# Optimization experiments

Measured on AMD Instinct MI355X. Metric: run time of the kernel, lower is better.

## Reference

```python
import jax, jax.numpy as jnp
import numpy as np

B, T, D = 2, 2048, 1024
H, KVH = 16, 4
HD = D // H            # 64
HALF = HD // 2         # 32
DFF = 4096
KW = 15
EPS = 1e-6


def zcrms(x, scale):
    # zero-centred RMSNorm: (1 + scale) * x / rms(x)
    rms = jnp.sqrt(jnp.mean(jnp.square(x.astype(jnp.float32)), axis=-1, keepdims=True) + EPS)
    return ((1.0 + scale) * x / rms).astype(x.dtype)


def apply_rope(x, cos, sin):
    # x: [B, H, T, HD]; cos/sin: [T, HALF]
    c = cos[None, None, :, :]
    s = sin[None, None, :, :]
    x1, x2 = x[..., :HALF], x[..., HALF:]
    return jnp.concatenate([x1 * c - x2 * s, x2 * c + x1 * s], axis=-1)


def setup_inputs() -> dict:
    key = jax.random.key(0)
    ks = jax.random.split(key, 20)
    std = 0.02
    inp = {
        "x": jax.random.normal(ks[0], (B, T, D), jnp.float32),
        "mask": jnp.ones((1, 1, T, T), dtype=bool),
        "cos": jnp.cos(jnp.arange(T, dtype=jnp.float32)[:, None]
                       * (10000.0 ** (-jnp.arange(HALF, dtype=jnp.float32) / HALF))[None, :]),
        "sin": jnp.sin(jnp.arange(T, dtype=jnp.float32)[:, None]
                       * (10000.0 ** (-jnp.arange(HALF, dtype=jnp.float32) / HALF))[None, :]),
        # attention
        "attn_norm_scale": jax.random.normal(ks[1], (D,), jnp.float32) * std,
        "q_kernel": jax.random.normal(ks[2], (D, D), jnp.float32) * std,
        "k_kernel": jax.random.normal(ks[3], (D, KVH * HD), jnp.float32) * std,
        "v_kernel": jax.random.normal(ks[4], (D, KVH * HD), jnp.float32) * std,
        "q_norm_scale": jax.random.normal(ks[5], (HD,), jnp.float32) * std,
        "k_norm_scale": jax.random.normal(ks[6], (HD,), jnp.float32) * std,
        "o_kernel": jax.random.normal(ks[7], (D, D), jnp.float32) * std,
        # conv module
        "conv_norm_scale": jax.random.normal(ks[8], (D,), jnp.float32) * std,
        "pw_up_kernel": jax.random.normal(ks[9], (D, 2 * D), jnp.float32) * std,
        "dw_kernel": jax.random.normal(ks[10], (KW, 1, D), jnp.float32) * std,
        "conv_inner_norm_scale": jax.random.normal(ks[11], (D,), jnp.float32) * std,
        "pw_down_kernel": jax.random.normal(ks[12], (D, D), jnp.float32) * std,
        # ffn
        "ffn_norm_scale": jax.random.normal(ks[13], (D,), jnp.float32) * std,
        "gate_kernel": jax.random.normal(ks[14], (D, DFF), jnp.float32) * std,
        "up_kernel": jax.random.normal(ks[15], (D, DFF), jnp.float32) * std,
        "down_kernel": jax.random.normal(ks[16], (DFF, D), jnp.float32) * std,
    }
    return inp


def reference(x, mask, cos, sin, attn_norm_scale, q_kernel, k_kernel, v_kernel,
              q_norm_scale, k_norm_scale, o_kernel, conv_norm_scale, pw_up_kernel,
              dw_kernel, conv_inner_norm_scale, pw_down_kernel, ffn_norm_scale,
              gate_kernel, up_kernel, down_kernel):
    # ---- pre-norm self-attention (GQA + QK-RMSNorm + RoPE) ----
    h = zcrms(x, attn_norm_scale)
    q = (h @ q_kernel).reshape(B, T, H, HD).transpose(0, 2, 1, 3)      # [B,H,T,HD]
    k = (h @ k_kernel).reshape(B, T, KVH, HD).transpose(0, 2, 1, 3)    # [B,KVH,T,HD]
    v = (h @ v_kernel).reshape(B, T, KVH, HD).transpose(0, 2, 1, 3)
    q = zcrms(q, q_norm_scale)
    k = zcrms(k, k_norm_scale)
    rep = H // KVH
    k = jnp.repeat(k, rep, axis=1)
    v = jnp.repeat(v, rep, axis=1)
    q = apply_rope(q, cos, sin)
    k = apply_rope(k, cos, sin)
    scale = jnp.sqrt(jnp.float32(HD))
    aw = jnp.einsum('bhqd,bhkd->bhqk', q, k) / scale
    aw = jnp.where(mask, aw, jnp.finfo(aw.dtype).min)
    aw = jax.nn.softmax(aw, axis=-1)
    attn = jnp.einsum('bhqk,bhkd->bhqd', aw, v).transpose(0, 2, 1, 3).reshape(B, T, D)
    x = x + attn @ o_kernel

    # ---- conformer conv module: pw_up -> GLU -> depthwise conv -> norm -> pw_down ----
    h = zcrms(x, conv_norm_scale)
    u = h @ pw_up_kernel
    u1, u2 = jnp.split(u, 2, axis=-1)
    g = u1 * jax.nn.sigmoid(u2)                                        # [B,T,D]
    c = jax.lax.conv_general_dilated(
        g, dw_kernel, window_strides=(1,), padding='SAME',
        feature_group_count=D, dimension_numbers=('NWC', 'WIO', 'NWC'))
    c = zcrms(c, conv_inner_norm_scale)
    x = x + c @ pw_down_kernel

    # ---- gated FFN with drelu activation ----
    h = zcrms(x, ffn_norm_scale)
    ff = jax.nn.relu(h @ gate_kernel) * jax.nn.relu(h @ up_kernel)
    x = x + ff @ down_kernel
    return x
```

## Files before the change

kernel.cpp:

```cpp
#include <hip/hip_runtime.h>


#define TT   2048
#define NTOK 4096

typedef __attribute__((ext_vector_type(8))) short short8;
typedef __attribute__((ext_vector_type(4))) float floatx4;

__device__ __forceinline__ unsigned short f2bf(float f) {
  unsigned int u = __float_as_uint(f);
  u = (u + 0x7fffu + ((u >> 16) & 1u)) >> 16;
  return (unsigned short)u;
}
__device__ __forceinline__ float bf2f(unsigned short s) {
  return __uint_as_float(((unsigned int)s) << 16);
}

__device__ __forceinline__ void glds16(const void* g, void* lds_base) {
  __builtin_amdgcn_global_load_lds(
      (const __attribute__((address_space(1))) void*)g,
      (__attribute__((address_space(3))) void*)lds_base, 16, 0, 0);
}

struct WJobs {
  const float* src[9];
  unsigned short* dst[9];
  int K[9], M[9], pm[9];
  int start[10];
};

__global__ __launch_bounds__(256) void wconv_all_kernel(WJobs tab) {
  int b = blockIdx.x;
  int j = 0;
  while (b >= tab.start[j + 1]) j++;
  int t = b - tab.start[j];
  const float* src = tab.src[j];
  unsigned short* dst = tab.dst[j];
  int K = tab.K[j], M = tab.M[j], pm = tab.pm[j];
  int mt = M >> 5;
  int m0 = (t % mt) * 32, k0 = (t / mt) * 32;
  int rowbase;
  if (pm == 0)      rowbase = m0;
  else if (pm == 1) rowbase = ((m0 & 1023) >> 5) * 64 + (m0 >> 10) * 32;
  else if (pm == 2) rowbase = (m0 >> 5) * 64;
  else              rowbase = (m0 >> 5) * 64 + 32;
  __shared__ float tile[32][33];
  int tx = threadIdx.x & 31, ty = threadIdx.x >> 5;
  for (int r = ty; r < 32; r += 8)
    tile[r][tx] = src[(size_t)(k0 + r) * M + m0 + tx];
  __syncthreads();
  for (int r = ty; r < 32; r += 8)
    dst[(size_t)(rowbase + r) * K + k0 + tx] = f2bf(tile[tx][r]);
}

template <bool BF16IN>
__global__ __launch_bounds__(256) void rmsnorm_kernel(
    const void* __restrict__ xin, const float* __restrict__ scale,
    unsigned short* __restrict__ out) {
  int t = blockIdx.x, tid = threadIdx.x;
  float xv[4];
  if (BF16IN) {
    ushort4 u = ((const ushort4*)((const unsigned short*)xin + (size_t)t * 1024))[tid];
    xv[0] = bf2f(u.x); xv[1] = bf2f(u.y); xv[2] = bf2f(u.z); xv[3] = bf2f(u.w);
  } else {
    float4 u = ((const float4*)((const float*)xin + (size_t)t * 1024))[tid];
    xv[0] = u.x; xv[1] = u.y; xv[2] = u.z; xv[3] = u.w;
  }
  float ss = xv[0] * xv[0] + xv[1] * xv[1] + xv[2] * xv[2] + xv[3] * xv[3];
#pragma unroll
  for (int off = 32; off > 0; off >>= 1) ss += __shfl_down(ss, off);
  __shared__ float red[4];
  if ((tid & 63) == 0) red[tid >> 6] = ss;
  __syncthreads();
  float rinv = rsqrtf((red[0] + red[1] + red[2] + red[3]) * (1.0f / 1024.0f) + 1e-6f);
  float4 sv = ((const float4*)scale)[tid];
  ushort4 o;
  o.x = f2bf((1.0f + sv.x) * xv[0] * rinv);
  o.y = f2bf((1.0f + sv.y) * xv[1] * rinv);
  o.z = f2bf((1.0f + sv.z) * xv[2] * rinv);
  o.w = f2bf((1.0f + sv.w) * xv[3] * rinv);
  ((ushort4*)(out + (size_t)t * 1024))[tid] = o;
}

template <int BN, int FUSE, int OUT, int RES>
__device__ __forceinline__ void gemm_body(
    const unsigned short* __restrict__ A, const unsigned short* __restrict__ Bt,
    void* __restrict__ Cout, const void* __restrict__ resid, int K, int M) {
  constexpr int NI = BN / 32;
  __shared__ __align__(16) unsigned short As[128 * 64];
  __shared__ __align__(16) unsigned short Bs[BN * 64];
  const int tid = threadIdx.x;
  const int wid = tid >> 6, lane = tid & 63;
  const int quad = lane >> 4, l16 = lane & 15;
  const int wm = (wid >> 1) * 64, wn = (wid & 1) * (BN / 2);

  int bx = blockIdx.x, by = blockIdx.y;
  if (gridDim.x == 16) {
    int pid = by * gridDim.x + bx;
    int inb = pid & 63, pidp = pid >> 6;
    by = (pidp & 3) * 8 + (inb & 7);
    bx = (pidp >> 2) * 8 + (inb >> 3);
  }
  const int row0 = by * 128;
  const int col0 = bx * BN;

  floatx4 acc[4][NI];
#pragma unroll
  for (int mi = 0; mi < 4; mi++)
#pragma unroll
    for (int ni = 0; ni < NI; ni++) acc[mi][ni] = (floatx4){0.f, 0.f, 0.f, 0.f};

  const unsigned short* Ag = A + (size_t)row0 * K;
  const unsigned short* Bg = Bt + (size_t)col0 * K;

  for (int k0 = 0; k0 < K; k0 += 64) {
#pragma unroll
    for (int j = 0; j < 4; j++) {
      int ci = tid + j * 256;
      int r = ci >> 3, c = (ci & 7) ^ (r & 7);
      glds16(Ag + (size_t)r * K + k0 + c * 8, &As[(wid * 64 + j * 256) * 8]);
    }
#pragma unroll
    for (int j = 0; j < BN / 32; j++) {
      int ci = tid + j * 256;
      int r = ci >> 3, c = (ci & 7) ^ (r & 7);
      glds16(Bg + (size_t)r * K + k0 + c * 8, &Bs[(wid * 64 + j * 256) * 8]);
    }
    __syncthreads();
#pragma unroll
    for (int kk = 0; kk < 64; kk += 32) {
      short8 a[4], b[NI];
#pragma unroll
      for (int mi = 0; mi < 4; mi++) {
        int r = wm + mi * 16 + l16;
        a[mi] = *(const short8*)&As[r * 64 + (((kk >> 3) + quad) ^ (r & 7)) * 8];
      }
#pragma unroll
      for (int ni = 0; ni < NI; ni++) {
        int r = wn + ni * 16 + l16;
        b[ni] = *(const short8*)&Bs[r * 64 + (((kk >> 3) + quad) ^ (r & 7)) * 8];
      }
#pragma unroll
      for (int mi = 0; mi < 4; mi++)
#pragma unroll
        for (int ni = 0; ni < NI; ni++)
          acc[mi][ni] = __builtin_amdgcn_mfma_f32_16x16x32_bf16(a[mi], b[ni], acc[mi][ni], 0, 0, 0);
    }
    __syncthreads();
  }

  if (FUSE == 0) {
#pragma unroll
    for (int mi = 0; mi < 4; mi++) {
#pragma unroll
      for (int reg = 0; reg < 4; reg++) {
        int grow = row0 + wm + mi * 16 + quad * 4 + reg;
#pragma unroll
        for (int ni = 0; ni < NI; ni++) {
          int gcol = col0 + wn + ni * 16 + l16;
          float v = acc[mi][ni][reg];
          if (RES == 1) v += ((const float*)resid)[(size_t)grow * M + gcol];
          if (RES == 2) v += bf2f(((const unsigned short*)resid)[(size_t)grow * M + gcol]);
          if (OUT == 1) ((unsigned short*)Cout)[(size_t)grow * M + gcol] = f2bf(v);
          else          ((float*)Cout)[(size_t)grow * M + gcol] = v;
        }
      }
    }
  } else {
    const int group = (col0 + wn) >> 6;
    const int MW = M >> 1;
#pragma unroll
    for (int mi = 0; mi < 4; mi++) {
#pragma unroll
      for (int reg = 0; reg < 4; reg++) {
        int grow = row0 + wm + mi * 16 + quad * 4 + reg;
#pragma unroll
        for (int ni = 0; ni < NI / 2; ni++) {
          int f = group * 32 + ni * 16 + l16;
          float a = acc[mi][ni][reg], b = acc[mi][ni + NI / 2][reg];
          float v;
          if (FUSE == 1) v = a / (1.0f + __expf(-b));
          else           v = fmaxf(a, 0.f) * fmaxf(b, 0.f);
          ((unsigned short*)Cout)[(size_t)grow * MW + f] = f2bf(v);
        }
      }
    }
  }
}

__global__ __launch_bounds__(256, 2) void gemm_oproj(
    const unsigned short* A, const unsigned short* Bt, void* C, const void* r, int K, int M) {
  gemm_body<64, 0, 1, 1>(A, Bt, C, r, K, M);
}
__global__ __launch_bounds__(256, 2) void gemm_glu(
    const unsigned short* A, const unsigned short* Bt, void* C, const void* r, int K, int M) {
  gemm_body<128, 1, 1, 0>(A, Bt, C, r, K, M);
}
__global__ __launch_bounds__(256, 2) void gemm_dn(
    const unsigned short* A, const unsigned short* Bt, void* C, const void* r, int K, int M) {
  gemm_body<64, 0, 1, 2>(A, Bt, C, r, K, M);
}
__global__ __launch_bounds__(256, 2) void gemm_gateup(
    const unsigned short* A, const unsigned short* Bt, void* C, const void* r, int K, int M) {
  gemm_body<128, 2, 1, 0>(A, Bt, C, r, K, M);
}
__global__ __launch_bounds__(256, 2) void gemm_ffdn(
    const unsigned short* A, const unsigned short* Bt, void* C, const void* r, int K, int M) {
  gemm_body<64, 0, 0, 2>(A, Bt, C, r, K, M);
}

#define QSCALE 0.180336880111f

__global__ __launch_bounds__(256, 2) void gemm_qkvf(
    const unsigned short* __restrict__ A, const unsigned short* __restrict__ Bt,
    const float* __restrict__ cosb, const float* __restrict__ sinb,
    const float* __restrict__ qns, const float* __restrict__ kns,
    unsigned short* __restrict__ qb, unsigned short* __restrict__ kb,
    unsigned short* __restrict__ vt) {
  constexpr int K = 1024;
  __shared__ __align__(16) unsigned short As[128 * 64];
  __shared__ __align__(16) unsigned short Bs[128 * 64];
  const int tid = threadIdx.x;
  const int wid = tid >> 6, lane = tid & 63;
  const int quad = lane >> 4, l16 = lane & 15;
  const int wm = (wid >> 1) * 64, wn = (wid & 1) * 64;
  const int row0 = blockIdx.y * 128;
  const int col0 = blockIdx.x * 128;

  floatx4 acc[4][4];
#pragma unroll
  for (int mi = 0; mi < 4; mi++)
#pragma unroll
    for (int ni = 0; ni < 4; ni++) acc[mi][ni] = (floatx4){0.f, 0.f, 0.f, 0.f};

  const unsigned short* Ag = A + (size_t)row0 * K;
  const unsigned short* Bg = Bt + (size_t)col0 * K;

  for (int k0 = 0; k0 < K; k0 += 64) {
#pragma unroll
    for (int j = 0; j < 4; j++) {
      int ci = tid + j * 256;
      int r = ci >> 3, c = (ci & 7) ^ (r & 7);
      glds16(Ag + (size_t)r * K + k0 + c * 8, &As[(wid * 64 + j * 256) * 8]);
      glds16(Bg + (size_t)r * K + k0 + c * 8, &Bs[(wid * 64 + j * 256) * 8]);
    }
    __syncthreads();
#pragma unroll
    for (int kk = 0; kk < 64; kk += 32) {
      short8 a[4], b[4];
#pragma unroll
      for (int mi = 0; mi < 4; mi++) {
        int r = wm + mi * 16 + l16;
        a[mi] = *(const short8*)&As[r * 64 + (((kk >> 3) + quad) ^ (r & 7)) * 8];
      }
#pragma unroll
      for (int ni = 0; ni < 4; ni++) {
        int r = wn + ni * 16 + l16;
        b[ni] = *(const short8*)&Bs[r * 64 + (((kk >> 3) + quad) ^ (r & 7)) * 8];
      }
#pragma unroll
      for (int mi = 0; mi < 4; mi++)
#pragma unroll
        for (int ni = 0; ni < 4; ni++)
          acc[mi][ni] = __builtin_amdgcn_mfma_f32_16x16x32_bf16(a[mi], b[ni], acc[mi][ni], 0, 0, 0);
    }
    __syncthreads();
  }

  const int head = (col0 + wn) >> 6;
  const int bi = row0 >> 11;

  if (head < 20) {
    const float* ns = (head < 16) ? qns : kns;
    float sc[4];
#pragma unroll
    for (int ni = 0; ni < 4; ni++) sc[ni] = 1.0f + ns[ni * 16 + l16];
#pragma unroll
    for (int mi = 0; mi < 4; mi++) {
#pragma unroll
      for (int reg = 0; reg < 4; reg++) {
        int row = row0 + wm + mi * 16 + quad * 4 + reg;
        int pos = row & (TT - 1);
        float ss = acc[mi][0][reg] * acc[mi][0][reg] + acc[mi][1][reg] * acc[mi][1][reg] +
                   acc[mi][2][reg] * acc[mi][2][reg] + acc[mi][3][reg] * acc[mi][3][reg];
        ss += __shfl_xor(ss, 1); ss += __shfl_xor(ss, 2);
        ss += __shfl_xor(ss, 4); ss += __shfl_xor(ss, 8);
        float rinv = rsqrtf(ss * (1.0f / 64.0f) + 1e-6f);
        float c0 = cosb[pos * 32 + l16],      s0 = sinb[pos * 32 + l16];
        float c1 = cosb[pos * 32 + 16 + l16], s1 = sinb[pos * 32 + 16 + l16];
        float nv0 = sc[0] * acc[mi][0][reg] * rinv;
        float nv1 = sc[1] * acc[mi][1][reg] * rinv;
        float nv2 = sc[2] * acc[mi][2][reg] * rinv;
        float nv3 = sc[3] * acc[mi][3][reg] * rinv;
        float o0 = nv0 * c0 - nv2 * s0;
        float o1 = nv1 * c1 - nv3 * s1;
        float o2 = nv2 * c0 + nv0 * s0;
        float o3 = nv3 * c1 + nv1 * s1;
        if (head < 16) {
          unsigned short* d = qb + (size_t)row * 1024 + head * 64 + l16;
          d[0] = f2bf(o0 * QSCALE); d[16] = f2bf(o1 * QSCALE);
          d[32] = f2bf(o2 * QSCALE); d[48] = f2bf(o3 * QSCALE);
        } else {
          unsigned short* d = kb + (size_t)row * 256 + (head - 16) * 64 + l16;
          d[0] = f2bf(o0); d[16] = f2bf(o1); d[32] = f2bf(o2); d[48] = f2bf(o3);
        }
      }
    }
  } else {
    const int g = bi * 4 + (head - 20);
    const int key0 = (row0 & (TT - 1)) + wm + quad * 4;
#pragma unroll
    for (int mi = 0; mi < 4; mi++) {
#pragma unroll
      for (int ni = 0; ni < 4; ni++) {
        int d = ni * 16 + l16;
        ushort4 pk;
        pk.x = f2bf(acc[mi][ni][0]); pk.y = f2bf(acc[mi][ni][1]);
        pk.z = f2bf(acc[mi][ni][2]); pk.w = f2bf(acc[mi][ni][3]);
        *(ushort4*)(vt + ((size_t)(g * 64 + d)) * TT + key0 + mi * 16) = pk;
      }
    }
  }
}

__global__ __launch_bounds__(512) void flash_kernel(
    const unsigned short* __restrict__ qb, const unsigned short* __restrict__ kb,
    const unsigned short* __restrict__ vt, unsigned short* __restrict__ ob) {
  const int qt = blockIdx.x;
  const int bh = blockIdx.y;
  const int bi = bh >> 4, h = bh & 15, kvh = h >> 2;
  const int tid = threadIdx.x, w = tid >> 6, lane = tid & 63;
  const int quad = lane >> 4, l16 = lane & 15;

  __shared__ __align__(16) unsigned short Ks[2][64 * 64];
  __shared__ __align__(16) unsigned short Vs[2][64 * 64];
  __shared__ __align__(16) unsigned short Ps[256 * 64];

  const unsigned short* qsrc = qb + ((size_t)(bi * TT + qt * 256)) * 1024 + h * 64;
  short8 qf[2][2];
#pragma unroll
  for (int af = 0; af < 2; af++) {
    const unsigned short* qr = qsrc + (size_t)(w * 32 + af * 16 + l16) * 1024;
    qf[af][0] = *(const short8*)(qr + quad * 8);
    qf[af][1] = *(const short8*)(qr + 32 + quad * 8);
  }

  const unsigned short* kbase = kb + ((size_t)(bi * TT)) * 256 + kvh * 64;
  const unsigned short* vbase = vt + ((size_t)(bi * 4 + kvh)) * (64 * TT);

  floatx4 oacc[2][4];
  floatx4 lacc[2];
#pragma unroll
  for (int af = 0; af < 2; af++) {
    lacc[af] = (floatx4){0.f, 0.f, 0.f, 0.f};
#pragma unroll
    for (int di = 0; di < 4; di++) oacc[af][di] = (floatx4){0.f, 0.f, 0.f, 0.f};
  }
  const short8 ones = (short8){0x3F80, 0x3F80, 0x3F80, 0x3F80,
                               0x3F80, 0x3F80, 0x3F80, 0x3F80};

  {
    int r = tid >> 3, c = (tid & 7) ^ (r & 7);
    glds16(kbase + (size_t)r * 256 + c * 8, &Ks[0][w * 512]);
    glds16(vbase + (size_t)r * TT + c * 8, &Vs[0][w * 512]);
  }

  for (int kt = 0; kt < 32; kt++) {
    const int buf = kt & 1;
    __syncthreads();
    if (kt < 31) {
      int r = tid >> 3, c = (tid & 7) ^ (r & 7);
      glds16(kbase + (size_t)((kt + 1) * 64 + r) * 256 + c * 8, &Ks[buf ^ 1][w * 512]);
      glds16(vbase + (size_t)r * TT + (kt + 1) * 64 + c * 8, &Vs[buf ^ 1][w * 512]);
    }

    short8 kf[4][2];
#pragma unroll
    for (int ni = 0; ni < 4; ni++) {
      int rb = ni * 16 + l16;
      kf[ni][0] = *(const short8*)&Ks[buf][rb * 64 + ((quad ^ (rb & 7)) * 8)];
      kf[ni][1] = *(const short8*)&Ks[buf][rb * 64 + (((4 + quad) ^ (rb & 7)) * 8)];
    }
#pragma unroll
    for (int af = 0; af < 2; af++) {
      const int rr = w * 32 + af * 16 + l16;
#pragma unroll
      for (int ni = 0; ni < 4; ni++) {
        floatx4 s = (floatx4){0.f, 0.f, 0.f, 0.f};
        s = __builtin_amdgcn_mfma_f32_16x16x32_bf16(kf[ni][0], qf[af][0], s, 0, 0, 0);
        s = __builtin_amdgcn_mfma_f32_16x16x32_bf16(kf[ni][1], qf[af][1], s, 0, 0, 0);
        union { unsigned short u[4]; unsigned long long ull; } pk;
#pragma unroll
        for (int r = 0; r < 4; r++)
          pk.u[r] = (unsigned short)(__float_as_uint(__builtin_amdgcn_exp2f(s[r])) >> 16);
        int ch = (ni * 2 + (quad >> 1)) ^ (rr & 7);
        *(unsigned long long*)&Ps[rr * 64 + ch * 8 + (quad & 1) * 4] = pk.ull;
      }
    }
    short8 vf[4][2];
#pragma unroll
    for (int di = 0; di < 4; di++) {
      int rb = di * 16 + l16;
      vf[di][0] = *(const short8*)&Vs[buf][rb * 64 + ((quad ^ (rb & 7)) * 8)];
      vf[di][1] = *(const short8*)&Vs[buf][rb * 64 + (((4 + quad) ^ (rb & 7)) * 8)];
    }
#pragma unroll
    for (int af = 0; af < 2; af++) {
      const int rr = w * 32 + af * 16 + l16;
      short8 pa0 = *(const short8*)&Ps[rr * 64 + ((quad ^ (rr & 7)) * 8)];
      short8 pa1 = *(const short8*)&Ps[rr * 64 + (((4 + quad) ^ (rr & 7)) * 8)];
      lacc[af] = __builtin_amdgcn_mfma_f32_16x16x32_bf16(pa0, ones, lacc[af], 0, 0, 0);
      lacc[af] = __builtin_amdgcn_mfma_f32_16x16x32_bf16(pa1, ones, lacc[af], 0, 0, 0);
#pragma unroll
      for (int di = 0; di < 4; di++) {
        oacc[af][di] = __builtin_amdgcn_mfma_f32_16x16x32_bf16(pa0, vf[di][0], oacc[af][di], 0, 0, 0);
        oacc[af][di] = __builtin_amdgcn_mfma_f32_16x16x32_bf16(pa1, vf[di][1], oacc[af][di], 0, 0, 0);
      }
    }
  }

  unsigned short* obase = ob + ((size_t)(bi * TT + qt * 256)) * 1024 + h * 64;
#pragma unroll
  for (int af = 0; af < 2; af++) {
    float rl[4];
#pragma unroll
    for (int r = 0; r < 4; r++) rl[r] = 1.0f / lacc[af][r];
#pragma unroll
    for (int di = 0; di < 4; di++)
#pragma unroll
      for (int r = 0; r < 4; r++) {
        int qrow = w * 32 + af * 16 + quad * 4 + r;
        obase[(size_t)qrow * 1024 + di * 16 + l16] = f2bf(oacc[af][di][r] * rl[r]);
      }
  }
}

__global__ __launch_bounds__(256) void convnorm_kernel(
    const unsigned short* __restrict__ g, const float* __restrict__ dw,
    const float* __restrict__ scale, unsigned short* __restrict__ out) {
  int tok = blockIdx.x;
  int bi = tok >> 11, pos = tok & (TT - 1);
  int tid = threadIdx.x, c0 = tid * 4;
  float a0 = 0.f, a1 = 0.f, a2 = 0.f, a3 = 0.f;
#pragma unroll
  for (int wk = 0; wk < 15; wk++) {
    int pp = pos + wk - 7;
    if (pp < 0 || pp >= TT) continue;
    ushort4 gv = *(const ushort4*)(g + ((size_t)(bi * TT + pp)) * 1024 + c0);
    float4 kv = *(const float4*)(dw + wk * 1024 + c0);
    a0 += bf2f(gv.x) * kv.x;
    a1 += bf2f(gv.y) * kv.y;
    a2 += bf2f(gv.z) * kv.z;
    a3 += bf2f(gv.w) * kv.w;
  }
  float ss = a0 * a0 + a1 * a1 + a2 * a2 + a3 * a3;
#pragma unroll
  for (int off = 32; off > 0; off >>= 1) ss += __shfl_down(ss, off);
  __shared__ float red[4];
  if ((tid & 63) == 0) red[tid >> 6] = ss;
  __syncthreads();
  float rinv = rsqrtf((red[0] + red[1] + red[2] + red[3]) * (1.0f / 1024.0f) + 1e-6f);
  float4 sv = *(const float4*)(scale + c0);
  ushort4 o;
  o.x = f2bf((1.0f + sv.x) * a0 * rinv);
  o.y = f2bf((1.0f + sv.y) * a1 * rinv);
  o.z = f2bf((1.0f + sv.z) * a2 * rinv);
  o.w = f2bf((1.0f + sv.w) * a3 * rinv);
  *(ushort4*)(out + (size_t)tok * 1024 + c0) = o;
}

extern "C" void kernel_launch(void* const* d_in, const int* in_sizes, int n_in,
                              void* d_out, int out_size, void* d_ws, size_t ws_size,
                              hipStream_t stream) {
  const float* x        = (const float*)d_in[0];
  const float* cosb     = (const float*)d_in[2];
  const float* sinb     = (const float*)d_in[3];
  const float* attn_ns  = (const float*)d_in[4];
  const float* qkern    = (const float*)d_in[5];
  const float* kkern    = (const float*)d_in[6];
  const float* vkern    = (const float*)d_in[7];
  const float* qns      = (const float*)d_in[8];
  const float* kns      = (const float*)d_in[9];
  const float* okern    = (const float*)d_in[10];
  const float* conv_ns  = (const float*)d_in[11];
  const float* pwupk    = (const float*)d_in[12];
  const float* dwk      = (const float*)d_in[13];
  const float* convi_ns = (const float*)d_in[14];
  const float* pwdnk    = (const float*)d_in[15];
  const float* ffn_ns   = (const float*)d_in[16];
  const float* gatek    = (const float*)d_in[17];
  const float* upk      = (const float*)d_in[18];
  const float* downk    = (const float*)d_in[19];
  float* out = (float*)d_out;
  char* ws = (char*)d_ws;

  const size_t O_QKVT = 0;
  const size_t O_OT   = O_QKVT + (size_t)1536 * 1024 * 2;
  const size_t O_UPT  = O_OT   + (size_t)1024 * 1024 * 2;
  const size_t O_DNT  = O_UPT  + (size_t)2048 * 1024 * 2;
  const size_t O_GUT  = O_DNT  + (size_t)1024 * 1024 * 2;
  const size_t O_DWNT = O_GUT  + (size_t)8192 * 1024 * 2;
  const size_t O_H    = O_DWNT + (size_t)4096 * 1024 * 2;
  const size_t O_BIG1 = O_H    + (size_t)4096 * 1024 * 2;
  const size_t O_QB   = O_BIG1 + (size_t)4096 * 8192 * 2;
  const size_t O_KB   = O_QB   + (size_t)4096 * 1024 * 2;
  const size_t O_VT   = O_KB   + (size_t)4096 * 256 * 2;
  const size_t O_ECN  = O_VT   + (size_t)8 * 64 * 2048 * 2;
  const size_t O_X1   = O_ECN  + (size_t)4096 * 1024 * 2;
  const size_t O_X2   = O_X1   + (size_t)4096 * 1024 * 2;
  const size_t O_BIG2 = O_X2   + (size_t)4096 * 1024 * 2;

  unsigned short* qkvT = (unsigned short*)(ws + O_QKVT);
  unsigned short* oT   = (unsigned short*)(ws + O_OT);
  unsigned short* upT  = (unsigned short*)(ws + O_UPT);
  unsigned short* dnT  = (unsigned short*)(ws + O_DNT);
  unsigned short* guT  = (unsigned short*)(ws + O_GUT);
  unsigned short* dwT  = (unsigned short*)(ws + O_DWNT);
  unsigned short* hbuf = (unsigned short*)(ws + O_H);
  unsigned short* big1u = (unsigned short*)(ws + O_BIG1);
  unsigned short* qbuf = (unsigned short*)(ws + O_QB);
  unsigned short* kbuf = (unsigned short*)(ws + O_KB);
  unsigned short* vtb  = (unsigned short*)(ws + O_VT);
  unsigned short* ecn  = (unsigned short*)(ws + O_ECN);
  unsigned short* x1b  = (unsigned short*)(ws + O_X1);
  unsigned short* x2b  = (unsigned short*)(ws + O_X2);
  unsigned short* big2 = (unsigned short*)(ws + O_BIG2);

  WJobs tab;
  tab.src[0] = qkern;  tab.dst[0] = qkvT;                       tab.K[0] = 1024; tab.M[0] = 1024; tab.pm[0] = 0;
  tab.src[1] = kkern;  tab.dst[1] = qkvT + (size_t)1024 * 1024; tab.K[1] = 1024; tab.M[1] = 256;  tab.pm[1] = 0;
  tab.src[2] = vkern;  tab.dst[2] = qkvT + (size_t)1280 * 1024; tab.K[2] = 1024; tab.M[2] = 256;  tab.pm[2] = 0;
  tab.src[3] = okern;  tab.dst[3] = oT;                         tab.K[3] = 1024; tab.M[3] = 1024; tab.pm[3] = 0;
  tab.src[4] = pwupk;  tab.dst[4] = upT;                        tab.K[4] = 1024; tab.M[4] = 2048; tab.pm[4] = 1;
  tab.src[5] = pwdnk;  tab.dst[5] = dnT;                        tab.K[5] = 1024; tab.M[5] = 1024; tab.pm[5] = 0;
  tab.src[6] = gatek;  tab.dst[6] = guT;                        tab.K[6] = 1024; tab.M[6] = 4096; tab.pm[6] = 2;
  tab.src[7] = upk;    tab.dst[7] = guT;                        tab.K[7] = 1024; tab.M[7] = 4096; tab.pm[7] = 3;
  tab.src[8] = downk;  tab.dst[8] = dwT;                        tab.K[8] = 4096; tab.M[8] = 1024; tab.pm[8] = 0;
  tab.start[0] = 0;
  for (int i = 0; i < 9; i++)
    tab.start[i + 1] = tab.start[i] + (tab.M[i] >> 5) * (tab.K[i] >> 5);
  wconv_all_kernel<<<tab.start[9], 256, 0, stream>>>(tab);

  rmsnorm_kernel<false><<<NTOK, 256, 0, stream>>>(x, attn_ns, hbuf);
  gemm_qkvf<<<dim3(12, 32), 256, 0, stream>>>(hbuf, qkvT, cosb, sinb, qns, kns,
                                              qbuf, kbuf, vtb);
  flash_kernel<<<dim3(8, 32), 512, 0, stream>>>(qbuf, kbuf, vtb, ecn);
  gemm_oproj<<<dim3(16, 32), 256, 0, stream>>>(ecn, oT, x1b, x, 1024, 1024);

  rmsnorm_kernel<true><<<NTOK, 256, 0, stream>>>(x1b, conv_ns, hbuf);
  gemm_glu<<<dim3(16, 32), 256, 0, stream>>>(hbuf, upT, big2, nullptr, 1024, 2048);
  convnorm_kernel<<<NTOK, 256, 0, stream>>>(big2, dwk, convi_ns, ecn);
  gemm_dn<<<dim3(16, 32), 256, 0, stream>>>(ecn, dnT, x2b, x1b, 1024, 1024);

  rmsnorm_kernel<true><<<NTOK, 256, 0, stream>>>(x2b, ffn_ns, hbuf);
  gemm_gateup<<<dim3(64, 32), 256, 0, stream>>>(hbuf, guT, big1u, nullptr, 1024, 8192);
  gemm_ffdn<<<dim3(16, 32), 256, 0, stream>>>(big1u, dwT, out, x2b, 4096, 1024);
}
```

Before: 457.6 us.

## Fold RMSNorm scales into weights and compute row norms in GEMM epilogues

```diff
diff --git a/kernel.cpp b/kernel.cpp
--- a/kernel.cpp
+++ b/kernel.cpp
@@ -24,6 +24,7 @@
 
 struct WJobs {
   const float* src[9];
+  const float* nsc[9];
   unsigned short* dst[9];
   int K[9], M[9], pm[9];
   int start[10];
@@ -35,6 +36,7 @@
   while (b >= tab.start[j + 1]) j++;
   int t = b - tab.start[j];
   const float* src = tab.src[j];
+  const float* nsc = tab.nsc[j];
   unsigned short* dst = tab.dst[j];
   int K = tab.K[j], M = tab.M[j], pm = tab.pm[j];
   int mt = M >> 5;
@@ -49,43 +51,38 @@
   for (int r = ty; r < 32; r += 8)
     tile[r][tx] = src[(size_t)(k0 + r) * M + m0 + tx];
   __syncthreads();
+  float ksc = nsc ? (1.0f + nsc[k0 + tx]) : 1.0f;
   for (int r = ty; r < 32; r += 8)
-    dst[(size_t)(rowbase + r) * K + k0 + tx] = f2bf(tile[tx][r]);
-}
-
-template <bool BF16IN>
-__global__ __launch_bounds__(256) void rmsnorm_kernel(
-    const void* __restrict__ xin, const float* __restrict__ scale,
-    unsigned short* __restrict__ out) {
+    dst[(size_t)(rowbase + r) * K + k0 + tx] = f2bf(tile[tx][r] * ksc);
+}
+
+__global__ __launch_bounds__(256) void prep_kernel(
+    const float* __restrict__ x, unsigned short* __restrict__ xb,
+    float* __restrict__ rinv1, float* __restrict__ sumsq2,
+    float* __restrict__ sumsq3) {
   int t = blockIdx.x, tid = threadIdx.x;
-  float xv[4];
-  if (BF16IN) {
-    ushort4 u = ((const ushort4*)((const unsigned short*)xin + (size_t)t * 1024))[tid];
-    xv[0] = bf2f(u.x); xv[1] = bf2f(u.y); xv[2] = bf2f(u.z); xv[3] = bf2f(u.w);
-  } else {
-    float4 u = ((const float4*)((const float*)xin + (size_t)t * 1024))[tid];
-    xv[0] = u.x; xv[1] = u.y; xv[2] = u.z; xv[3] = u.w;
-  }
-  float ss = xv[0] * xv[0] + xv[1] * xv[1] + xv[2] * xv[2] + xv[3] * xv[3];
+  float4 xv = ((const float4*)(x + (size_t)t * 1024))[tid];
+  float ss = xv.x * xv.x + xv.y * xv.y + xv.z * xv.z + xv.w * xv.w;
 #pragma unroll
   for (int off = 32; off > 0; off >>= 1) ss += __shfl_down(ss, off);
   __shared__ float red[4];
   if ((tid & 63) == 0) red[tid >> 6] = ss;
   __syncthreads();
-  float rinv = rsqrtf((red[0] + red[1] + red[2] + red[3]) * (1.0f / 1024.0f) + 1e-6f);
-  float4 sv = ((const float4*)scale)[tid];
+  float tot = red[0] + red[1] + red[2] + red[3];
+  if (tid == 0) rinv1[t] = rsqrtf(tot * (1.0f / 1024.0f) + 1e-6f);
   ushort4 o;
-  o.x = f2bf((1.0f + sv.x) * xv[0] * rinv);
-  o.y = f2bf((1.0f + sv.y) * xv[1] * rinv);
-  o.z = f2bf((1.0f + sv.z) * xv[2] * rinv);
-  o.w = f2bf((1.0f + sv.w) * xv[3] * rinv);
-  ((ushort4*)(out + (size_t)t * 1024))[tid] = o;
-}
-
-template <int BN, int FUSE, int OUT, int RES>
+  o.x = f2bf(xv.x); o.y = f2bf(xv.y); o.z = f2bf(xv.z); o.w = f2bf(xv.w);
+  ((ushort4*)(xb + (size_t)t * 1024))[tid] = o;
+  if (t < 16)       sumsq2[t * 256 + tid] = 0.f;
+  else if (t < 32)  sumsq3[(t - 16) * 256 + tid] = 0.f;
+}
+
+template <int BN, int FUSE, int OUT, int RES, int RSC, bool SQO>
 __device__ __forceinline__ void gemm_body(
     const unsigned short* __restrict__ A, const unsigned short* __restrict__ Bt,
-    void* __restrict__ Cout, const void* __restrict__ resid, int K, int M) {
+    void* __restrict__ Cout, const void* __restrict__ resid,
+    const float* __restrict__ ssq_in, float* __restrict__ ssq_out,
+    int K, int M) {
   constexpr int NI = BN / 32;
   __shared__ __align__(16) unsigned short As[128 * 64];
   __shared__ __align__(16) unsigned short Bs[BN * 64];
@@ -155,15 +152,21 @@
 #pragma unroll
       for (int reg = 0; reg < 4; reg++) {
         int grow = row0 + wm + mi * 16 + quad * 4 + reg;
+        float sq = 0.f;
 #pragma unroll
         for (int ni = 0; ni < NI; ni++) {
           int gcol = col0 + wn + ni * 16 + l16;
           float v = acc[mi][ni][reg];
-          if (RES == 1) v += ((const float*)resid)[(size_t)grow * M + gcol];
           if (RES == 2) v += bf2f(((const unsigned short*)resid)[(size_t)grow * M + gcol]);
+          if (SQO) sq += v * v;
           if (OUT == 1) ((unsigned short*)Cout)[(size_t)grow * M + gcol] = f2bf(v);
           else          ((float*)Cout)[(size_t)grow * M + gcol] = v;
         }
+        if (SQO) {
+          sq += __shfl_xor(sq, 1); sq += __shfl_xor(sq, 2);
+          sq += __shfl_xor(sq, 4); sq += __shfl_xor(sq, 8);
+          if (l16 == 0) atomicAdd(&ssq_out[grow], sq);
+        }
       }
     }
   } else {
@@ -174,13 +177,15 @@
 #pragma unroll
       for (int reg = 0; reg < 4; reg++) {
         int grow = row0 + wm + mi * 16 + quad * 4 + reg;
+        float r = 1.f;
+        if (RSC) r = rsqrtf(ssq_in[grow] * (1.0f / 1024.0f) + 1e-6f);
 #pragma unroll
         for (int ni = 0; ni < NI / 2; ni++) {
           int f = group * 32 + ni * 16 + l16;
           float a = acc[mi][ni][reg], b = acc[mi][ni + NI / 2][reg];
           float v;
-          if (FUSE == 1) v = a / (1.0f + __expf(-b));
-          else           v = fmaxf(a, 0.f) * fmaxf(b, 0.f);
+          if (FUSE == 1) { a *= r; b *= r; v = a / (1.0f + __expf(-b)); }
+          else           { v = r * r * fmaxf(a, 0.f) * fmaxf(b, 0.f); }
           ((unsigned short*)Cout)[(size_t)grow * MW + f] = f2bf(v);
         }
       }
@@ -189,24 +194,29 @@
 }
 
 __global__ __launch_bounds__(256, 2) void gemm_oproj(
-    const unsigned short* A, const unsigned short* Bt, void* C, const void* r, int K, int M) {
-  gemm_body<64, 0, 1, 1>(A, Bt, C, r, K, M);
+    const unsigned short* A, const unsigned short* Bt, void* C, const void* r,
+    const float* si, float* so, int K, int M) {
+  gemm_body<64, 0, 1, 2, 0, true>(A, Bt, C, r, si, so, K, M);
 }
 __global__ __launch_bounds__(256, 2) void gemm_glu(
-    const unsigned short* A, const unsigned short* Bt, void* C, const void* r, int K, int M) {
-  gemm_body<128, 1, 1, 0>(A, Bt, C, r, K, M);
+    const unsigned short* A, const unsigned short* Bt, void* C, const void* r,
+    const float* si, float* so, int K, int M) {
+  gemm_body<128, 1, 1, 0, 1, false>(A, Bt, C, r, si, so, K, M);
 }
 __global__ __launch_bounds__(256, 2) void gemm_dn(
-    const unsigned short* A, const unsigned short* Bt, void* C, const void* r, int K, int M) {
-  gemm_body<64, 0, 1, 2>(A, Bt, C, r, K, M);
+    const unsigned short* A, const unsigned short* Bt, void* C, const void* r,
+    const float* si, float* so, int K, int M) {
+  gemm_body<64, 0, 1, 2, 0, true>(A, Bt, C, r, si, so, K, M);
 }
 __global__ __launch_bounds__(256, 2) void gemm_gateup(
-    const unsigned short* A, const unsigned short* Bt, void* C, const void* r, int K, int M) {
-  gemm_body<128, 2, 1, 0>(A, Bt, C, r, K, M);
+    const unsigned short* A, const unsigned short* Bt, void* C, const void* r,
+    const float* si, float* so, int K, int M) {
+  gemm_body<128, 2, 1, 0, 2, false>(A, Bt, C, r, si, so, K, M);
 }
 __global__ __launch_bounds__(256, 2) void gemm_ffdn(
-    const unsigned short* A, const unsigned short* Bt, void* C, const void* r, int K, int M) {
-  gemm_body<64, 0, 0, 2>(A, Bt, C, r, K, M);
+    const unsigned short* A, const unsigned short* Bt, void* C, const void* r,
+    const float* si, float* so, int K, int M) {
+  gemm_body<64, 0, 0, 2, 0, false>(A, Bt, C, r, si, so, K, M);
 }
 
 #define QSCALE 0.180336880111f
@@ -215,8 +225,8 @@
     const unsigned short* __restrict__ A, const unsigned short* __restrict__ Bt,
     const float* __restrict__ cosb, const float* __restrict__ sinb,
     const float* __restrict__ qns, const float* __restrict__ kns,
-    unsigned short* __restrict__ qb, unsigned short* __restrict__ kb,
-    unsigned short* __restrict__ vt) {
+    const float* __restrict__ rinv1, unsigned short* __restrict__ qb,
+    unsigned short* __restrict__ kb, unsigned short* __restrict__ vt) {
   constexpr int K = 1024;
   __shared__ __align__(16) unsigned short As[128 * 64];
   __shared__ __align__(16) unsigned short Bs[128 * 64];
@@ -311,19 +321,21 @@
     const int key0 = (row0 & (TT - 1)) + wm + quad * 4;
 #pragma unroll
     for (int mi = 0; mi < 4; mi++) {
+      int rb = row0 + wm + mi * 16 + quad * 4;
+      float r0 = rinv1[rb], r1 = rinv1[rb + 1], r2 = rinv1[rb + 2], r3 = rinv1[rb + 3];
 #pragma unroll
       for (int ni = 0; ni < 4; ni++) {
         int d = ni * 16 + l16;
         ushort4 pk;
-        pk.x = f2bf(acc[mi][ni][0]); pk.y = f2bf(acc[mi][ni][1]);
-        pk.z = f2bf(acc[mi][ni][2]); pk.w = f2bf(acc[mi][ni][3]);
+        pk.x = f2bf(acc[mi][ni][0] * r0); pk.y = f2bf(acc[mi][ni][1] * r1);
+        pk.z = f2bf(acc[mi][ni][2] * r2); pk.w = f2bf(acc[mi][ni][3] * r3);
         *(ushort4*)(vt + ((size_t)(g * 64 + d)) * TT + key0 + mi * 16) = pk;
       }
     }
   }
 }
 
-__global__ __launch_bounds__(512) void flash_kernel(
+__global__ __launch_bounds__(256) void flash_kernel(
     const unsigned short* __restrict__ qb, const unsigned short* __restrict__ kb,
     const unsigned short* __restrict__ vt, unsigned short* __restrict__ ob) {
   const int qt = blockIdx.x;
@@ -334,9 +346,9 @@
 
   __shared__ __align__(16) unsigned short Ks[2][64 * 64];
   __shared__ __align__(16) unsigned short Vs[2][64 * 64];
-  __shared__ __align__(16) unsigned short Ps[256 * 64];
-
-  const unsigned short* qsrc = qb + ((size_t)(bi * TT + qt * 256)) * 1024 + h * 64;
+  __shared__ __align__(16) unsigned short Ps[128 * 64];
+
+  const unsigned short* qsrc = qb + ((size_t)(bi * TT + qt * 128)) * 1024 + h * 64;
   short8 qf[2][2];
 #pragma unroll
   for (int af = 0; af < 2; af++) {
@@ -360,18 +372,28 @@
                                0x3F80, 0x3F80, 0x3F80, 0x3F80};
 
   {
-    int r = tid >> 3, c = (tid & 7) ^ (r & 7);
-    glds16(kbase + (size_t)r * 256 + c * 8, &Ks[0][w * 512]);
-    glds16(vbase + (size_t)r * TT + c * 8, &Vs[0][w * 512]);
+#pragma unroll
+    for (int j = 0; j < 2; j++) {
+      int ci = tid + j * 256;
+      int r = ci >> 3, c = (ci & 7) ^ (r & 7);
+      glds16(kbase + (size_t)r * 256 + c * 8, &Ks[0][(w * 64 + j * 256) * 8]);
+      glds16(vbase + (size_t)r * TT + c * 8, &Vs[0][(w * 64 + j * 256) * 8]);
+    }
   }
 
   for (int kt = 0; kt < 32; kt++) {
     const int buf = kt & 1;
     __syncthreads();
     if (kt < 31) {
-      int r = tid >> 3, c = (tid & 7) ^ (r & 7);
-      glds16(kbase + (size_t)((kt + 1) * 64 + r) * 256 + c * 8, &Ks[buf ^ 1][w * 512]);
-      glds16(vbase + (size_t)r * TT + (kt + 1) * 64 + c * 8, &Vs[buf ^ 1][w * 512]);
+#pragma unroll
+      for (int j = 0; j < 2; j++) {
+        int ci = tid + j * 256;
+        int r = ci >> 3, c = (ci & 7) ^ (r & 7);
+        glds16(kbase + (size_t)((kt + 1) * 64 + r) * 256 + c * 8,
+               &Ks[buf ^ 1][(w * 64 + j * 256) * 8]);
+        glds16(vbase + (size_t)r * TT + (kt + 1) * 64 + c * 8,
+               &Vs[buf ^ 1][(w * 64 + j * 256) * 8]);
+      }
     }
 
     short8 kf[4][2];
@@ -419,7 +441,7 @@
     }
   }
 
-  unsigned short* obase = ob + ((size_t)(bi * TT + qt * 256)) * 1024 + h * 64;
+  unsigned short* obase = ob + ((size_t)(bi * TT + qt * 128)) * 1024 + h * 64;
 #pragma unroll
   for (int af = 0; af < 2; af++) {
     float rl[4];
@@ -500,8 +522,8 @@
   const size_t O_DNT  = O_UPT  + (size_t)2048 * 1024 * 2;
   const size_t O_GUT  = O_DNT  + (size_t)1024 * 1024 * 2;
   const size_t O_DWNT = O_GUT  + (size_t)8192 * 1024 * 2;
-  const size_t O_H    = O_DWNT + (size_t)4096 * 1024 * 2;
-  const size_t O_BIG1 = O_H    + (size_t)4096 * 1024 * 2;
+  const size_t O_XB   = O_DWNT + (size_t)4096 * 1024 * 2;
+  const size_t O_BIG1 = O_XB   + (size_t)4096 * 1024 * 2;
   const size_t O_QB   = O_BIG1 + (size_t)4096 * 8192 * 2;
   const size_t O_KB   = O_QB   + (size_t)4096 * 1024 * 2;
   const size_t O_VT   = O_KB   + (size_t)4096 * 256 * 2;
@@ -509,6 +531,9 @@
   const size_t O_X1   = O_ECN  + (size_t)4096 * 1024 * 2;
   const size_t O_X2   = O_X1   + (size_t)4096 * 1024 * 2;
   const size_t O_BIG2 = O_X2   + (size_t)4096 * 1024 * 2;
+  const size_t O_RV1  = O_BIG2 + (size_t)4096 * 1024 * 2;
+  const size_t O_SS2  = O_RV1  + (size_t)4096 * 4;
+  const size_t O_SS3  = O_SS2  + (size_t)4096 * 4;
 
   unsigned short* qkvT = (unsigned short*)(ws + O_QKVT);
   unsigned short* oT   = (unsigned short*)(ws + O_OT);
@@ -516,7 +541,7 @@
   unsigned short* dnT  = (unsigned short*)(ws + O_DNT);
   unsigned short* guT  = (unsigned short*)(ws + O_GUT);
   unsigned short* dwT  = (unsigned short*)(ws + O_DWNT);
-  unsigned short* hbuf = (unsigned short*)(ws + O_H);
+  unsigned short* xb   = (unsigned short*)(ws + O_XB);
   unsigned short* big1u = (unsigned short*)(ws + O_BIG1);
   unsigned short* qbuf = (unsigned short*)(ws + O_QB);
   unsigned short* kbuf = (unsigned short*)(ws + O_KB);
@@ -525,34 +550,40 @@
   unsigned short* x1b  = (unsigned short*)(ws + O_X1);
   unsigned short* x2b  = (unsigned short*)(ws + O_X2);
   unsigned short* big2 = (unsigned short*)(ws + O_BIG2);
+  float*          rinv1 = (float*)(ws + O_RV1);
+  float*          sumsq2 = (float*)(ws + O_SS2);
+  float*          sumsq3 = (float*)(ws + O_SS3);
 
   WJobs tab;
-  tab.src[0] = qkern;  tab.dst[0] = qkvT;                       tab.K[0] = 1024; tab.M[0] = 1024; tab.pm[0] = 0;
-  tab.src[1] = kkern;  tab.dst[1] = qkvT + (size_t)1024 * 1024; tab.K[1] = 1024; tab.M[1] = 256;  tab.pm[1] = 0;
-  tab.src[2] = vkern;  tab.dst[2] = qkvT + (size_t)1280 * 1024; tab.K[2] = 1024; tab.M[2] = 256;  tab.pm[2] = 0;
-  tab.src[3] = okern;  tab.dst[3] = oT;                         tab.K[3] = 1024; tab.M[3] = 1024; tab.pm[3] = 0;
-  tab.src[4] = pwupk;  tab.dst[4] = upT;                        tab.K[4] = 1024; tab.M[4] = 2048; tab.pm[4] = 1;
-  tab.src[5] = pwdnk;  tab.dst[5] = dnT;                        tab.K[5] = 1024; tab.M[5] = 1024; tab.pm[5] = 0;
-  tab.src[6] = gatek;  tab.dst[6] = guT;                        tab.K[6] = 1024; tab.M[6] = 4096; tab.pm[6] = 2;
-  tab.src[7] = upk;    tab.dst[7] = guT;                        tab.K[7] = 1024; tab.M[7] = 4096; tab.pm[7] = 3;
-  tab.src[8] = downk;  tab.dst[8] = dwT;                        tab.K[8] = 4096; tab.M[8] = 1024; tab.pm[8] = 0;
+  tab.src[0] = qkern;  tab.nsc[0] = attn_ns; tab.dst[0] = qkvT;                       tab.K[0] = 1024; tab.M[0] = 1024; tab.pm[0] = 0;
+  tab.src[1] = kkern;  tab.nsc[1] = attn_ns; tab.dst[1] = qkvT + (size_t)1024 * 1024; tab.K[1] = 1024; tab.M[1] = 256;  tab.pm[1] = 0;
+  tab.src[2] = vkern;  tab.nsc[2] = attn_ns; tab.dst[2] = qkvT + (size_t)1280 * 1024; tab.K[2] = 1024; tab.M[2] = 256;  tab.pm[2] = 0;
+  tab.src[3] = okern;  tab.nsc[3] = nullptr; tab.dst[3] = oT;                         tab.K[3] = 1024; tab.M[3] = 1024; tab.pm[3] = 0;
+  tab.src[4] = pwupk;  tab.nsc[4] = conv_ns; tab.dst[4] = upT;                        tab.K[4] = 1024; tab.M[4] = 2048; tab.pm[4] = 1;
+  tab.src[5] = pwdnk;  tab.nsc[5] = nullptr; tab.dst[5] = dnT;                        tab.K[5] = 1024; tab.M[5] = 1024; tab.pm[5] = 0;
+  tab.src[6] = gatek;  tab.nsc[6] = ffn_ns;  tab.dst[6] = guT;                        tab.K[6] = 1024; tab.M[6] = 4096; tab.pm[6] = 2;
+  tab.src[7] = upk;    tab.nsc[7] = ffn_ns;  tab.dst[7] = guT;                        tab.K[7] = 1024; tab.M[7] = 4096; tab.pm[7] = 3;
+  tab.src[8] = downk;  tab.nsc[8] = nullptr; tab.dst[8] = dwT;                        tab.K[8] = 4096; tab.M[8] = 1024; tab.pm[8] = 0;
   tab.start[0] = 0;
   for (int i = 0; i < 9; i++)
     tab.start[i + 1] = tab.start[i] + (tab.M[i] >> 5) * (tab.K[i] >> 5);
   wconv_all_kernel<<<tab.start[9], 256, 0, stream>>>(tab);
 
-  rmsnorm_kernel<false><<<NTOK, 256, 0, stream>>>(x, attn_ns, hbuf);
-  gemm_qkvf<<<dim3(12, 32), 256, 0, stream>>>(hbuf, qkvT, cosb, sinb, qns, kns,
-                                              qbuf, kbuf, vtb);
-  flash_kernel<<<dim3(8, 32), 512, 0, stream>>>(qbuf, kbuf, vtb, ecn);
-  gemm_oproj<<<dim3(16, 32), 256, 0, stream>>>(ecn, oT, x1b, x, 1024, 1024);
-
-  rmsnorm_kernel<true><<<NTOK, 256, 0, stream>>>(x1b, conv_ns, hbuf);
-  gemm_glu<<<dim3(16, 32), 256, 0, stream>>>(hbuf, upT, big2, nullptr, 1024, 2048);
+  prep_kernel<<<NTOK, 256, 0, stream>>>(x, xb, rinv1, sumsq2, sumsq3);
+  gemm_qkvf<<<dim3(12, 32), 256, 0, stream>>>(xb, qkvT, cosb, sinb, qns, kns,
+                                              rinv1, qbuf, kbuf, vtb);
+  flash_kernel<<<dim3(16, 32), 256, 0, stream>>>(qbuf, kbuf, vtb, ecn);
+  gemm_oproj<<<dim3(16, 32), 256, 0, stream>>>(ecn, oT, x1b, xb, nullptr, sumsq2,
+                                               1024, 1024);
+
+  gemm_glu<<<dim3(16, 32), 256, 0, stream>>>(x1b, upT, big2, nullptr, sumsq2,
+                                             nullptr, 1024, 2048);
   convnorm_kernel<<<NTOK, 256, 0, stream>>>(big2, dwk, convi_ns, ecn);
-  gemm_dn<<<dim3(16, 32), 256, 0, stream>>>(ecn, dnT, x2b, x1b, 1024, 1024);
-
-  rmsnorm_kernel<true><<<NTOK, 256, 0, stream>>>(x2b, ffn_ns, hbuf);
-  gemm_gateup<<<dim3(64, 32), 256, 0, stream>>>(hbuf, guT, big1u, nullptr, 1024, 8192);
-  gemm_ffdn<<<dim3(16, 32), 256, 0, stream>>>(big1u, dwT, out, x2b, 4096, 1024);
-}
+  gemm_dn<<<dim3(16, 32), 256, 0, stream>>>(ecn, dnT, x2b, x1b, nullptr, sumsq3,
+                                            1024, 1024);
+
+  gemm_gateup<<<dim3(64, 32), 256, 0, stream>>>(x2b, guT, big1u, nullptr, sumsq3,
+                                                nullptr, 1024, 8192);
+  gemm_ffdn<<<dim3(16, 32), 256, 0, stream>>>(big1u, dwT, out, x2b, nullptr,
+                                              nullptr, 4096, 1024);
+}
```

Result: slower. 486.8 us (+6.4%).
